# Optimization experiments

Hardware: AMD Instinct MI355X
Metric: run time of the kernel (lower is better)

Reference implementation:

```python
import jax, jax.numpy as jnp
import numpy as np

B, N = 32, 2048
EMBED = 64  # embed_dim -> channels 2 -> 64 -> 128 -> 256


def setup_inputs() -> dict:
    key = jax.random.key(0)
    ks = jax.random.split(key, 4)
    points = jax.random.normal(ks[0], (B, N, 2), dtype=jnp.float32)
    # Glorot-ish scaled weights (GCNConv lin has no bias; separate additive bias)
    W1 = jax.random.normal(ks[1], (2, EMBED), dtype=jnp.float32) * (1.0 / np.sqrt(2))
    W2 = jax.random.normal(ks[2], (EMBED, 2 * EMBED), dtype=jnp.float32) * (1.0 / np.sqrt(EMBED))
    W3 = jax.random.normal(ks[3], (2 * EMBED, 4 * EMBED), dtype=jnp.float32) * (1.0 / np.sqrt(2 * EMBED))
    b1 = jnp.zeros((EMBED,), dtype=jnp.float32)
    b2 = jnp.zeros((2 * EMBED,), dtype=jnp.float32)
    b3 = jnp.zeros((4 * EMBED,), dtype=jnp.float32)
    return {"points": points, "W1": W1, "b1": b1, "W2": W2, "b2": b2, "W3": W3, "b3": b3}


def _norm_adj(p):
    # p: [N, 2]. torch.cdist p=2, then threshold < 1.0 (includes diagonal, dist=0).
    n2 = jnp.sum(p * p, axis=-1)  # [N]
    d2 = n2[:, None] + n2[None, :] - 2.0 * (p @ p.T)
    dist = jnp.sqrt(jnp.maximum(d2, 0.0))
    A = (dist < 1.0).astype(jnp.float32)
    # PyG GCNConv adds self-loops on top of existing ones -> diagonal weight 2
    A = A + jnp.eye(p.shape[0], dtype=jnp.float32)
    deg = jnp.sum(A, axis=1)  # symmetric, >= 2 so no div-by-zero
    dinv = 1.0 / jnp.sqrt(deg)
    return A * dinv[:, None] * dinv[None, :]  # D^-1/2 (A+I) D^-1/2


def reference(points, W1, b1, W2, b2, W3, b3):
    def single(p):
        An = _norm_adj(p)  # [N, N]
        h = jax.nn.relu(An @ (p @ W1) + b1)
        h = jax.nn.relu(An @ (h @ W2) + b2)
        h = An @ (h @ W3) + b3
        return h  # [N, 4*EMBED]

    return jax.vmap(single)(points)  # [B, N, 4*EMBED]
```

## Files before the change

kernel.cpp:

```cpp
#include <hip/hip_runtime.h>
#include <hip/hip_bf16.h>
#include <cstdint>
#include <cstddef>

#define BATCH 32
#define NPTS  2048
#define NFLAT (BATCH * NPTS)
#define MROWS 32

typedef __attribute__((ext_vector_type(8))) short bf16x8;
typedef __attribute__((ext_vector_type(4))) short bf16x4;
typedef __attribute__((ext_vector_type(4))) float f32x4;
typedef __attribute__((ext_vector_type(16))) float f32x16;

__device__ inline unsigned short f2b(float v) {
    __hip_bfloat16 h = __float2bfloat16(v);
    return __builtin_bit_cast(unsigned short, h);
}

__device__ inline void gl_lds16(const void* g, void* l) {
    __builtin_amdgcn_global_load_lds(
        (const __attribute__((address_space(1))) unsigned int*)g,
        (__attribute__((address_space(3))) unsigned int*)l, 16, 0, 0);
}

#define OFF_DINV 0
#define OFF_MASK 262144
#define OFF_G1   17039360
#define OFF_G2   50593792
#define OFF_WB   67371008

__global__ __launch_bounds__(256) void k_cvtW2(const float* __restrict__ W2,
                                               const float* __restrict__ W3,
                                               unsigned short* __restrict__ Wp2,
                                               unsigned short* __restrict__ Wp3) {
    int i = blockIdx.x * 256 + threadIdx.x;
    if (i < 64 * 128) {
        int k = i >> 7, c = i & 127;
        size_t off = (((size_t)(k >> 4) * 4 + (c >> 5)) * 64
                      + ((((k >> 3) & 1) << 5) | (c & 31))) * 8 + (k & 7);
        Wp2[off] = f2b(W2[i]);
    }
    {
        int k = i >> 8, c = i & 255;
        size_t off = (((size_t)(k >> 4) * 8 + (c >> 5)) * 64
                      + ((((k >> 3) & 1) << 5) | (c & 31))) * 8 + (k & 7);
        Wp3[off] = f2b(W3[i]);
    }
}

__global__ __launch_bounds__(256) void k_mask(const float* __restrict__ pts,
                                              float* __restrict__ dinv,
                                              uint32_t* __restrict__ maskT) {
    const int b = blockIdx.y;
    const int row0 = blockIdx.x * MROWS;
    const int tid = threadIdx.x, lane = tid & 63, wv = tid >> 6;
    __shared__ float px[2112], py[2112];
    __shared__ uint32_t tb[64][MROWS + 1];
    const float2* P = (const float2*)(pts + (size_t)b * NPTS * 2);
    for (int j = tid; j < NPTS; j += 256) {
        float2 p = P[j];
        px[j + (j >> 5)] = p.x; py[j + (j >> 5)] = p.y;
    }
    __syncthreads();
    const int base = 33 * lane;
    for (int rr = 0; rr < MROWS / 4; ++rr) {
        const int il = wv * (MROWS / 4) + rr;
        const int i = row0 + il;
        const float xi = px[i + (i >> 5)], yi = py[i + (i >> 5)];
        uint32_t bits = 0;
        #pragma unroll
        for (int t = 0; t < 32; ++t) {
            float dx = xi - px[base + t], dy = yi - py[base + t];
            bits |= (dx * dx + dy * dy < 1.0f) ? (1u << t) : 0u;
        }
        tb[lane][il] = bits;
        int cnt = __popc(bits);
        #pragma unroll
        for (int off = 32; off; off >>= 1) cnt += __shfl_xor(cnt, off);
        if (lane == 0) dinv[b * NPTS + i] = rsqrtf((float)(cnt + 1));
    }
    __syncthreads();
    const int w = tid >> 2, il0 = (tid & 3) * 8;
    uint32_t* dst = maskT + ((size_t)b * 64 + w) * NPTS + row0 + il0;
    #pragma unroll
    for (int e = 0; e < 8; ++e) dst[e] = tb[w][il0 + e];
}

__global__ __launch_bounds__(256) void k_l1m(const float* __restrict__ pts,
                                             const float* __restrict__ W1,
                                             const float* __restrict__ b1,
                                             const float* __restrict__ dinv,
                                             const uint32_t* __restrict__ maskT,
                                             unsigned short* __restrict__ G1) {
    const int lid = blockIdx.x;
    const int g = (lid & 7) * 64 + (lid >> 3);
    const int b = g >> 4;
    const int row0 = (g & 15) * 128;
    const int tid = threadIdx.x;
    const int lane = tid & 63, wv = tid >> 6;
    const int l15 = lane & 15, lg = lane >> 4;

    __shared__ uint32_t Ms[64][128];
    __shared__ unsigned short Ubf[NPTS], Vbf[NPTS];
    __shared__ alignas(128) unsigned short LUT4[64];
    __shared__ float sdinv[128];

    if (tid < 16) {
        ushort4 e;
        e.x = (tid & 1) ? 0x3F80 : 0; e.y = (tid & 2) ? 0x3F80 : 0;
        e.z = (tid & 4) ? 0x3F80 : 0; e.w = (tid & 8) ? 0x3F80 : 0;
        *(ushort4*)&LUT4[tid * 4] = e;
    }
    if (tid < 128) sdinv[tid] = dinv[b * NPTS + row0 + tid];
    {
        const float2* P = (const float2*)(pts + (size_t)b * NPTS * 2);
        const float* dvp = dinv + (size_t)b * NPTS;
        const int j0 = tid * 8;
        #pragma unroll
        for (int e = 0; e < 8; ++e) {
            float d = dvp[j0 + e]; float2 p = P[j0 + e];
            Ubf[j0 + e] = f2b(d * p.x); Vbf[j0 + e] = f2b(d * p.y);
        }
    }
    {
        const uint32_t* msrc = maskT + (size_t)b * 64 * NPTS + row0;
        #pragma unroll
        for (int k = 0; k < 8; ++k) {
            int idx = tid + k * 256;
            int w = idx >> 5, c4 = idx & 31;
            *(uint4*)&Ms[w][c4 * 4] = *(const uint4*)(msrc + (size_t)w * NPTS + c4 * 4);
        }
    }
    __syncthreads();

    f32x4 acc0 = (f32x4){0.f, 0.f, 0.f, 0.f};
    f32x4 acc1 = (f32x4){0.f, 0.f, 0.f, 0.f};
    const int lrow = wv * 32 + l15;
    const bf16x8 zb = (bf16x8){0, 0, 0, 0, 0, 0, 0, 0};

    for (int kt = 0; kt < 64; ++kt) {
        bf16x8 ub = *(const bf16x8*)&Ubf[kt * 32 + lg * 8];
        bf16x8 vb = *(const bf16x8*)&Vbf[kt * 32 + lg * 8];
        bf16x8 bf = (l15 == 0) ? ub : ((l15 == 1) ? vb : zb);
        #pragma unroll
        for (int mf = 0; mf < 2; ++mf) {
            const int row = row0 + lrow + mf * 16;
            uint32_t mw = Ms[kt][lrow + mf * 16];
            uint32_t by = (mw >> (lg * 8)) & 0xffu;
            bf16x4 lo = *(const bf16x4*)&LUT4[(by & 15u) * 4];
            bf16x4 hi = *(const bf16x4*)&LUT4[(by >> 4) * 4];
            bf16x8 af = __builtin_shufflevector(lo, hi, 0, 1, 2, 3, 4, 5, 6, 7);
            if (kt == (row >> 5)) {
                int e = (row & 31) - lg * 8;
                #pragma unroll
                for (int e2 = 0; e2 < 8; ++e2)
                    if (e2 == e) af[e2] = (short)0x4000;
            }
            if (mf == 0) acc0 = __builtin_amdgcn_mfma_f32_16x16x32_bf16(af, bf, acc0, 0, 0, 0);
            else         acc1 = __builtin_amdgcn_mfma_f32_16x16x32_bf16(af, bf, acc1, 0, 0, 0);
        }
    }

    float w1x[4], w1y[4], bb4[4];
    #pragma unroll
    for (int g4 = 0; g4 < 4; ++g4) {
        w1x[g4] = W1[l15 + 16 * g4];
        w1y[g4] = W1[64 + l15 + 16 * g4];
        bb4[g4] = b1[l15 + 16 * g4];
    }
    #pragma unroll
    for (int mf = 0; mf < 2; ++mf) {
        const int ks1 = mf | ((wv & 1) << 1);
        const int kt1 = (row0 >> 6) + (wv >> 1);
        #pragma unroll
        for (int r = 0; r < 4; ++r) {
            float av = (mf == 0) ? acc0[r] : acc1[r];
            float sx = __shfl(av, (lane & 48));
            float sy = __shfl(av, (lane & 48) | 1);
            const int rloc = wv * 32 + mf * 16 + lg * 4 + r;
            const float di = sdinv[rloc];
            const int e1 = (lg * 4 + r) & 7;
            const int kh1 = lg >> 1;
            #pragma unroll
            for (int g4 = 0; g4 < 4; ++g4) {
                float h = fmaxf(di * (sx * w1x[g4] + sy * w1y[g4]) + bb4[g4], 0.f);
                size_t off = ((((size_t)(b * 32 + kt1) * 2 + (g4 >> 1)) * 4 + ks1) * 512)
                             + (size_t)((kh1 << 5) | (l15 + 16 * (g4 & 1))) * 8 + e1;
                G1[off] = f2b(di * h);
            }
        }
    }
}

template<int CIN, int COUT, bool RELU, bool F32OUT>
__global__ __launch_bounds__(256, 2) void k_gcnF(const uint32_t* __restrict__ maskT,
                                                 const float* __restrict__ dinv,
                                                 const unsigned short* __restrict__ G,
                                                 const unsigned short* __restrict__ Wp,
                                                 const float* __restrict__ bias,
                                                 void* __restrict__ outp) {
    constexpr int BM = 128;
    constexpr int NF = CIN / 64;
    const int lid = blockIdx.x;
    const int g = (lid & 7) * 64 + (lid >> 3);
    const int b = g >> 4;
    const int row0 = (g & 15) * BM;
    const int tid = threadIdx.x;
    const int lane = tid & 63, wv = tid >> 6;
    const int wm = wv >> 1, wn = wv & 1;
    const int l31 = lane & 31, lg2 = lane >> 5;

    __shared__ alignas(16) unsigned short YsZ[128 * (CIN + 4)];
    __shared__ uint32_t Ms[64][BM];
    __shared__ alignas(128) unsigned short LUT4[64];
    __shared__ float sdinv[BM];

    if (tid < 16) {
        ushort4 e;
        e.x = (tid & 1) ? 0x3F80 : 0; e.y = (tid & 2) ? 0x3F80 : 0;
        e.z = (tid & 4) ? 0x3F80 : 0; e.w = (tid & 8) ? 0x3F80 : 0;
        *(ushort4*)&LUT4[tid * 4] = e;
    }
    if (tid < BM) sdinv[tid] = dinv[b * NPTS + row0 + tid];
    {
        const uint32_t* msrc = maskT + (size_t)b * 64 * NPTS + row0;
        #pragma unroll
        for (int k = 0; k < 8; ++k) {
            int idx = tid + k * 256;
            int w = idx >> 5, c4 = idx & 31;
            *(uint4*)&Ms[w][c4 * 4] = *(const uint4*)(msrc + (size_t)w * NPTS + c4 * 4);
        }
    }

    f32x16 acc[2][NF];
    #pragma unroll
    for (int mf = 0; mf < 2; ++mf)
        #pragma unroll
        for (int nf = 0; nf < NF; ++nf)
            #pragma unroll
            for (int r = 0; r < 16; ++r)
                acc[mf][nf][r] = 0.f;

    const int ktd = (row0 >> 6) + wm;
    const int arow = wm * 64 + l31;

    for (int kt = 0; kt < NPTS / 64; ++kt) {
        const unsigned short* ysrc = G + (size_t)(b * 32 + kt) * (CIN / 32) * 2048;
        #pragma unroll
        for (int q = 0; q < CIN / 32; ++q) {
            int fi = wv * (CIN / 32) + q;
            gl_lds16(ysrc + (size_t)fi * 512 + lane * 8, (char*)YsZ + fi * 1024);
        }
        asm volatile("s_waitcnt vmcnt(0)" ::: "memory");
        __syncthreads();

        uint32_t M[2][2];
        #pragma unroll
        for (int mf = 0; mf < 2; ++mf)
            #pragma unroll
            for (int q = 0; q < 2; ++q)
                M[mf][q] = Ms[kt * 2 + q][arow + mf * 32];

        #pragma unroll
        for (int ks = 0; ks < 4; ++ks) {
            bf16x8 af[2];
            #pragma unroll
            for (int mf = 0; mf < 2; ++mf) {
                uint32_t by = (M[mf][ks >> 1] >> (((ks & 1) * 2 + lg2) * 8)) & 0xffu;
                bf16x4 lo = *(const bf16x4*)&LUT4[(by & 15u) * 4];
                bf16x4 hi = *(const bf16x4*)&LUT4[(by >> 4) * 4];
                af[mf] = __builtin_shufflevector(lo, hi, 0, 1, 2, 3, 4, 5, 6, 7);
            }
            if (kt == ktd) {
                #pragma unroll
                for (int mf = 0; mf < 2; ++mf) {
                    int e = mf * 32 + l31 - ks * 16 - lg2 * 8;
                    #pragma unroll
                    for (int e2 = 0; e2 < 8; ++e2)
                        if (e2 == e) af[mf][e2] = (short)0x4000;
                }
            }
            #pragma unroll
            for (int nf = 0; nf < NF; ++nf) {
                bf16x8 bf = *(const bf16x8*)((const char*)YsZ
                            + ((((wn * NF + nf) * 4 + ks) * 64 + lane) << 4));
                #pragma unroll
                for (int mf = 0; mf < 2; ++mf)
                    acc[mf][nf] = __builtin_amdgcn_mfma_f32_32x32x16_bf16(af[mf], bf, acc[mf][nf], 0, 0, 0);
            }
        }
        __syncthreads();
    }

    #pragma unroll
    for (int mf = 0; mf < 2; ++mf)
        #pragma unroll
        for (int nf = 0; nf < NF; ++nf) {
            const int col = wn * (CIN / 2) + nf * 32 + l31;
            #pragma unroll
            for (int reg = 0; reg < 16; ++reg) {
                const int row = wm * 64 + mf * 32 + (reg & 3) + 8 * (reg >> 2) + 4 * lg2;
                YsZ[row * (CIN + 4) + col] = f2b(acc[mf][nf][reg]);
            }
        }
    __syncthreads();

    f32x16 acc2[2][COUT / 64];
    #pragma unroll
    for (int amf = 0; amf < 2; ++amf)
        #pragma unroll
        for (int cnf = 0; cnf < COUT / 64; ++cnf)
            #pragma unroll
            for (int r = 0; r < 16; ++r)
                acc2[amf][cnf][r] = 0.f;

    #pragma unroll
    for (int kq = 0; kq < CIN / 16; ++kq) {
        bf16x8 za[2];
        #pragma unroll
        for (int amf = 0; amf < 2; ++amf)
            za[amf] = *(const bf16x8*)&YsZ[(wm * 64 + amf * 32 + l31) * (CIN + 4) + kq * 16 + lg2 * 8];
        #pragma unroll
        for (int cnf = 0; cnf < COUT / 64; ++cnf) {
            const int cblk = wn * (COUT / 64) + cnf;
            bf16x8 wf = *(const bf16x8*)(Wp + ((size_t)(kq * (COUT / 32) + cblk) * 64 + lane) * 8);
            #pragma unroll
            for (int amf = 0; amf < 2; ++amf)
                acc2[amf][cnf] = __builtin_amdgcn_mfma_f32_32x32x16_bf16(za[amf], wf, acc2[amf][cnf], 0, 0, 0);
        }
    }

    #pragma unroll
    for (int amf = 0; amf < 2; ++amf) {
        #pragma unroll
        for (int cnf = 0; cnf < COUT / 64; ++cnf) {
            const int col = wn * (COUT / 2) + cnf * 32 + l31;
            const float bb = bias[col];
            #pragma unroll
            for (int reg = 0; reg < 16; ++reg) {
                const int row = wm * 64 + amf * 32 + (reg & 3) + 8 * (reg >> 2) + 4 * lg2;
                const float di = sdinv[row];
                float h = di * acc2[amf][cnf][reg] + bb;
                if (RELU) h = fmaxf(h, 0.f);
                if (F32OUT) {
                    ((float*)outp)[((size_t)(b * NPTS + row0 + row)) * COUT + col] = h;
                } else {
                    const int j = row0 + row;
                    const int kt1 = j >> 6, ks1 = (j >> 4) & 3, kh1 = (j >> 3) & 1, e1 = j & 7;
                    size_t off = ((((size_t)(b * 32 + kt1) * (COUT / 32) + (col >> 5)) * 4 + ks1) * 512)
                                 + (size_t)((kh1 << 5) | (col & 31)) * 8 + e1;
                    ((unsigned short*)outp)[off] = f2b(di * h);
                }
            }
        }
    }
}

extern "C" void kernel_launch(void* const* d_in, const int* in_sizes, int n_in,
                              void* d_out, int out_size, void* d_ws, size_t ws_size,
                              hipStream_t stream) {
    const float* pts = (const float*)d_in[0];
    const float* W1  = (const float*)d_in[1];
    const float* b1  = (const float*)d_in[2];
    const float* W2  = (const float*)d_in[3];
    const float* b2  = (const float*)d_in[4];
    const float* W3  = (const float*)d_in[5];
    const float* b3  = (const float*)d_in[6];

    char* ws = (char*)d_ws;
    float*          dinv  = (float*)(ws + OFF_DINV);
    uint32_t*       maskT = (uint32_t*)(ws + OFF_MASK);
    unsigned short* G1    = (unsigned short*)(ws + OFF_G1);
    unsigned short* G2    = (unsigned short*)(ws + OFF_G2);
    unsigned short* Wp2   = (unsigned short*)(ws + OFF_WB);
    unsigned short* Wp3   = Wp2 + 64 * 128;
    float* out = (float*)d_out;

    k_cvtW2<<<dim3(128), dim3(256), 0, stream>>>(W2, W3, Wp2, Wp3);
    k_mask<<<dim3(NPTS / MROWS, BATCH), dim3(256), 0, stream>>>(pts, dinv, maskT);
    k_l1m<<<dim3(512), dim3(256), 0, stream>>>(pts, W1, b1, dinv, maskT, G1);
    k_gcnF<64, 128, true, false><<<dim3(512), dim3(256), 0, stream>>>(maskT, dinv, G1, Wp2, b2, G2);
    k_gcnF<128, 256, false, true><<<dim3(512), dim3(256), 0, stream>>>(maskT, dinv, G2, Wp3, b3, out);
}
```

Before: 135.2 us.

## Double-buffer feature tiles in LDS to overlap global loads with MFMA

The GCN aggregation loop now stages the next K-tile of features into a second LDS buffer while the current tile is consumed by MFMAs, using partial vmcnt waits and raw s_barrier instead of a full wait plus syncthreads each iteration. The shared buffer is enlarged to hold two tiles when that exceeds the epilogue staging size. This hides global-to-LDS load latency, at the cost of more LDS per block, which may reduce occupancy, and of delicate wait-count correctness.

```diff
diff --git a/kernel.cpp b/kernel.cpp
--- a/kernel.cpp
+++ b/kernel.cpp
@@ -202,6 +202,7 @@
                                                  void* __restrict__ outp) {
     constexpr int BM = 128;
     constexpr int NF = CIN / 64;
+    constexpr int LSZ = (2 * CIN * 64 > 128 * (CIN + 4)) ? 2 * CIN * 64 : 128 * (CIN + 4);
     const int lid = blockIdx.x;
     const int g = (lid & 7) * 64 + (lid >> 3);
     const int b = g >> 4;
@@ -211,7 +212,7 @@
     const int wm = wv >> 1, wn = wv & 1;
     const int l31 = lane & 31, lg2 = lane >> 5;
 
-    __shared__ alignas(16) unsigned short YsZ[128 * (CIN + 4)];
+    __shared__ alignas(16) unsigned short YsZ[LSZ];
     __shared__ uint32_t Ms[64][BM];
     __shared__ alignas(128) unsigned short LUT4[64];
     __shared__ float sdinv[BM];
@@ -245,23 +246,23 @@
     const int ktd = (row0 >> 6) + wm;
     const int arow = wm * 64 + l31;
 
-    for (int kt = 0; kt < NPTS / 64; ++kt) {
+    auto stage = [&](int buf, int kt) {
         const unsigned short* ysrc = G + (size_t)(b * 32 + kt) * (CIN / 32) * 2048;
         #pragma unroll
         for (int q = 0; q < CIN / 32; ++q) {
             int fi = wv * (CIN / 32) + q;
-            gl_lds16(ysrc + (size_t)fi * 512 + lane * 8, (char*)YsZ + fi * 1024);
-        }
-        asm volatile("s_waitcnt vmcnt(0)" ::: "memory");
-        __syncthreads();
-
+            gl_lds16(ysrc + (size_t)fi * 512 + lane * 8,
+                     (char*)YsZ + buf * (CIN * 128) + fi * 1024);
+        }
+    };
+    auto body = [&](int buf, int kt) {
+        const char* ybase = (const char*)YsZ + buf * (CIN * 128);
         uint32_t M[2][2];
         #pragma unroll
         for (int mf = 0; mf < 2; ++mf)
             #pragma unroll
             for (int q = 0; q < 2; ++q)
                 M[mf][q] = Ms[kt * 2 + q][arow + mf * 32];
-
         #pragma unroll
         for (int ks = 0; ks < 4; ++ks) {
             bf16x8 af[2];
@@ -283,14 +284,34 @@
             }
             #pragma unroll
             for (int nf = 0; nf < NF; ++nf) {
-                bf16x8 bf = *(const bf16x8*)((const char*)YsZ
+                bf16x8 bf = *(const bf16x8*)(ybase
                             + ((((wn * NF + nf) * 4 + ks) * 64 + lane) << 4));
                 #pragma unroll
                 for (int mf = 0; mf < 2; ++mf)
                     acc[mf][nf] = __builtin_amdgcn_mfma_f32_32x32x16_bf16(af[mf], bf, acc[mf][nf], 0, 0, 0);
             }
         }
-        __syncthreads();
+    };
+
+    __syncthreads();
+    stage(0, 0);
+    for (int kt = 0; kt < 32; kt += 2) {
+        stage(1, kt + 1);
+        if constexpr (CIN == 128) asm volatile("s_waitcnt vmcnt(4)" ::: "memory");
+        else                      asm volatile("s_waitcnt vmcnt(2)" ::: "memory");
+        __builtin_amdgcn_s_barrier();
+        body(0, kt);
+        __builtin_amdgcn_s_barrier();
+        if (kt + 2 < 32) {
+            stage(0, kt + 2);
+            if constexpr (CIN == 128) asm volatile("s_waitcnt vmcnt(4)" ::: "memory");
+            else                      asm volatile("s_waitcnt vmcnt(2)" ::: "memory");
+        } else {
+            asm volatile("s_waitcnt vmcnt(0)" ::: "memory");
+        }
+        __builtin_amdgcn_s_barrier();
+        body(1, kt + 1);
+        __builtin_amdgcn_s_barrier();
     }
 
     #pragma unroll
```

Result: faster. 128.3 us, median of 2 (-5.1%).
